# Kernel optimization log

Hardware: AMD Instinct MI355X
Metric: run time of the kernel (lower is better)

## Reference

```python
import jax, jax.numpy as jnp
import numpy as np

B, V, D = 128, 1024, 512

def setup_inputs() -> dict:
    key = jax.random.key(0)
    ks = jax.random.split(key, 6)
    return {
        "features": jax.random.normal(ks[0], (B, D), dtype=jnp.float32),
        "phoneme_counts": jax.random.uniform(ks[1], (V,), minval=0.01, maxval=1.0, dtype=jnp.float32),
        "total_count": jnp.asarray(float(V), dtype=jnp.float32),
        "meg_prototypes": jax.random.normal(ks[2], (V, D), dtype=jnp.float32),
        "zipf_s": jnp.asarray(1.0, dtype=jnp.float32),
        "temperature": jnp.asarray(1.0, dtype=jnp.float32),
        "W1": jax.random.normal(ks[3], (D, 2 * D), dtype=jnp.float32) * 0.02,
        "b1": jnp.zeros((D,), dtype=jnp.float32),
        "W2": jax.random.normal(ks[4], (1, D), dtype=jnp.float32) * 0.02,
        "b2": jnp.zeros((1,), dtype=jnp.float32),
    }

def _l2norm(x, axis=-1, eps=1e-12):
    n = jnp.sqrt(jnp.sum(x * x, axis=axis, keepdims=True))
    return x / jnp.maximum(n, eps)

def reference(features, phoneme_counts, total_count, meg_prototypes,
              zipf_s, temperature, W1, b1, W2, b2):
    vocab = phoneme_counts.shape[0]
    d = features.shape[1]
    # Zipf weights: rank phonemes by frequency (descending), weight = rank^{-s}
    freqs = phoneme_counts / jnp.maximum(total_count, 1.0)
    order = jnp.argsort(-freqs)  # indices sorted by descending frequency
    ranks = jnp.zeros_like(freqs).at[order].set(
        jnp.arange(1, vocab + 1, dtype=freqs.dtype))
    zw = jnp.power(jnp.maximum(ranks, 1.0), -zipf_s)
    zipf_priors = zw / jnp.maximum(zw.sum(), 1e-8)  # [V]
    # Cosine similarity / temperature
    sim = _l2norm(features) @ _l2norm(meg_prototypes).T  # [B, V]
    sim = sim / jnp.maximum(temperature, 1e-4)
    # MLP attention: split Linear(2D,D) into feature and prototype halves,
    # avoiding the materialized [B,V,2D] concat.
    Wf, Wp = W1[:, :d], W1[:, d:]  # each [D, D]
    feat_part = features @ Wf.T          # [B, D]
    proto_part = meg_prototypes @ Wp.T   # [V, D]
    h = jax.nn.relu(feat_part[:, None, :] + proto_part[None, :, :] + b1)  # [B, V, D]
    attn = jax.nn.sigmoid(jnp.einsum('bvd,d->bv', h, W2[0]) + b2[0])      # [B, V]
    weights = zipf_priors[None, :] * (1.0 + sim) * attn
    return jax.nn.softmax(weights, axis=-1)
```

## Files before the change

kernel.cpp:

```cpp
#include <hip/hip_runtime.h>
#include <hip/hip_bf16.h>


typedef __attribute__((ext_vector_type(8))) short bhalf8;
typedef __attribute__((ext_vector_type(4))) float f32x4;

static __device__ __forceinline__ unsigned short f2bf(float x) {
    union { __hip_bfloat16 h; unsigned short u; } cv;
    cv.h = __float2bfloat16(x);
    return cv.u;
}

static __device__ __forceinline__ float bf2f(unsigned short u) {
    return __uint_as_float(((unsigned int)u) << 16);
}

static __device__ __forceinline__ int4 pack_bf16_8(float4 x, float4 y) {
    union { ushort u[8]; int4 v; } r;
    r.u[0] = f2bf(x.x); r.u[1] = f2bf(x.y); r.u[2] = f2bf(x.z); r.u[3] = f2bf(x.w);
    r.u[4] = f2bf(y.x); r.u[5] = f2bf(y.y); r.u[6] = f2bf(y.z); r.u[7] = f2bf(y.w);
    return r.v;
}

__global__ __launch_bounds__(256) void gemm_prep_kernel(
    const float* __restrict__ feat, const float* __restrict__ counts,
    const float* __restrict__ proto, const float* __restrict__ zs,
    const float* __restrict__ W1, const float* __restrict__ b1,
    float* __restrict__ fpT, unsigned short* __restrict__ ppbT,
    float* __restrict__ dotraw,
    float* __restrict__ zw, float* __restrict__ invf, float* __restrict__ invp)
{
    int bx = blockIdx.x, tid = threadIdx.x;

    __shared__ unsigned short As[2][64 * 72];
    __shared__ unsigned short Bs[2][64 * 72];

    if (bx >= 176) {
        if (bx < 192) {
            float* cn = (float*)&As[0][0];
            ((float4*)cn)[tid] = ((const float4*)counts)[tid];
            __syncthreads();
            int il = tid >> 2, q = tid & 3;
            int i = (bx - 176) * 64 + il;
            float ci = cn[i];
            int cnt = 0;
            int j0 = q * 256;
            for (int j = j0; j < j0 + 256; ++j) {
                float cj = cn[j];
                cnt += (cj > ci) ? 1 : 0;
                cnt += (cj == ci && j < i) ? 1 : 0;
            }
            cnt += __shfl_xor(cnt, 1);
            cnt += __shfl_xor(cnt, 2);
            if (q == 0) zw[i] = powf((float)(cnt + 1), -zs[0]);
        } else {
            int nb = bx - 192;
            int w = tid >> 6, lane = tid & 63;
            int row = nb * 4 + w;
            const float* src = (row < 128) ? (feat + (size_t)row * 512)
                                           : (proto + (size_t)(row - 128) * 512);
            const float4* rp = (const float4*)src;
            float4 a = rp[lane * 2], b = rp[lane * 2 + 1];
            float ss = a.x*a.x + a.y*a.y + a.z*a.z + a.w*a.w
                     + b.x*b.x + b.y*b.y + b.z*b.z + b.w*b.w;
            for (int o = 32; o; o >>= 1) ss += __shfl_xor(ss, o);
            if (lane == 0) {
                float inv = 1.0f / fmaxf(sqrtf(ss), 1e-12f);
                if (row < 128) invf[row] = inv; else invp[row - 128] = inv;
            }
        }
        return;
    }

    const float* A; const float* Bm;
    int lda, ldb, tm, tn, mode;
    if (bx < 16) {
        A = feat; lda = 512; Bm = W1; ldb = 1024; mode = 0;
        tm = bx >> 3; tn = bx & 7;
    } else if (bx < 144) {
        int t = bx - 16;
        A = W1 + 512; lda = 1024; Bm = proto; ldb = 512; mode = 1;
        tm = t >> 4; tn = t & 15;
    } else {
        int t = bx - 144;
        A = feat; lda = 512; Bm = proto; ldb = 512; mode = 2;
        tm = t >> 4; tn = t & 15;
    }

    int r = tid >> 2, kq = (tid & 3) * 16;
    int wave = tid >> 6, lane = tid & 63;
    int fr = lane & 15, quad = lane >> 4;

    const float* Ag = A + (size_t)(tm * 64 + r) * lda + kq;
    const float* Bg = Bm + (size_t)(tn * 64 + r) * ldb + kq;

    float4 a0 = *(const float4*)(Ag),      a1 = *(const float4*)(Ag + 4);
    float4 a2 = *(const float4*)(Ag + 8),  a3 = *(const float4*)(Ag + 12);
    float4 g0 = *(const float4*)(Bg),      g1 = *(const float4*)(Bg + 4);
    float4 g2 = *(const float4*)(Bg + 8),  g3 = *(const float4*)(Bg + 12);

    f32x4 acc0 = {0.f, 0.f, 0.f, 0.f};
    f32x4 acc1 = acc0, acc2 = acc0, acc3 = acc0;

    for (int kc = 0; kc < 512; kc += 64) {
        int p = (kc >> 6) & 1;
        *(int4*)&As[p][r * 72 + kq]     = pack_bf16_8(a0, a1);
        *(int4*)&As[p][r * 72 + kq + 8] = pack_bf16_8(a2, a3);
        *(int4*)&Bs[p][r * 72 + kq]     = pack_bf16_8(g0, g1);
        *(int4*)&Bs[p][r * 72 + kq + 8] = pack_bf16_8(g2, g3);
        __syncthreads();
        if (kc + 64 < 512) {
            const float* An = Ag + kc + 64;
            const float* Bn = Bg + kc + 64;
            a0 = *(const float4*)(An);     a1 = *(const float4*)(An + 4);
            a2 = *(const float4*)(An + 8); a3 = *(const float4*)(An + 12);
            g0 = *(const float4*)(Bn);     g1 = *(const float4*)(Bn + 4);
            g2 = *(const float4*)(Bn + 8); g3 = *(const float4*)(Bn + 12);
        }
        #pragma unroll
        for (int s = 0; s < 2; ++s) {
            int ko = s * 32 + quad * 8;
            bhalf8 af  = *(const bhalf8*)&As[p][(wave * 16 + fr) * 72 + ko];
            bhalf8 bf0 = *(const bhalf8*)&Bs[p][(fr) * 72 + ko];
            bhalf8 bf1 = *(const bhalf8*)&Bs[p][(16 + fr) * 72 + ko];
            bhalf8 bf2 = *(const bhalf8*)&Bs[p][(32 + fr) * 72 + ko];
            bhalf8 bf3 = *(const bhalf8*)&Bs[p][(48 + fr) * 72 + ko];
            acc0 = __builtin_amdgcn_mfma_f32_16x16x32_bf16(af, bf0, acc0, 0, 0, 0);
            acc1 = __builtin_amdgcn_mfma_f32_16x16x32_bf16(af, bf1, acc1, 0, 0, 0);
            acc2 = __builtin_amdgcn_mfma_f32_16x16x32_bf16(af, bf2, acc2, 0, 0, 0);
            acc3 = __builtin_amdgcn_mfma_f32_16x16x32_bf16(af, bf3, acc3, 0, 0, 0);
        }
    }

    int m0 = tm * 64 + wave * 16 + quad * 4;
    int n0 = tn * 64 + fr;
    f32x4 accs[4] = {acc0, acc1, acc2, acc3};
    if (mode == 0) {
        for (int j = 0; j < 4; ++j)
            for (int rr = 0; rr < 4; ++rr)
                fpT[(size_t)(n0 + j * 16) * 128 + m0 + rr] = accs[j][rr];
    } else if (mode == 1) {
        float bv4[4];
        for (int rr = 0; rr < 4; ++rr) bv4[rr] = b1[m0 + rr];
        for (int j = 0; j < 4; ++j)
            for (int rr = 0; rr < 4; ++rr)
                ppbT[(size_t)(m0 + rr) * 1024 + n0 + j * 16] = f2bf(accs[j][rr] + bv4[rr]);
    } else {
        for (int j = 0; j < 4; ++j)
            for (int rr = 0; rr < 4; ++rr)
                dotraw[(size_t)(m0 + rr) * 1024 + n0 + j * 16] = accs[j][rr];
    }
}

__global__ __launch_bounds__(1024) void head_kernel(
    const float* __restrict__ fpT, const unsigned short* __restrict__ ppbT,
    const float* __restrict__ dotraw, const float* __restrict__ zw,
    const float* __restrict__ invf, const float* __restrict__ invp,
    const float* __restrict__ temp, const float* __restrict__ W2,
    const float* __restrict__ b2, float* __restrict__ out)
{
    int b = blockIdx.x, tid = threadIdx.x;
    int wave = tid >> 6, lane = tid & 63;
    int vt = tid & 255, ks = tid >> 8;
    int v4 = vt * 4, k0 = ks * 128;

    __shared__ float hpart[4 * 1024];
    __shared__ float red[16];

    float h0 = 0.f, h1 = 0.f, h2 = 0.f, h3 = 0.f;
    const unsigned short* pc = ppbT + v4;
    #pragma unroll 8
    for (int k = k0; k < k0 + 128; ++k) {
        ushort2 u2 = *(const ushort2*)(pc + ((size_t)k << 10));
        unsigned int ua = ((const unsigned int*)&u2)[0];
        unsigned int ub = ((const unsigned int*)&u2)[1];
        float p0 = __uint_as_float(ua << 16);
        float p1 = __uint_as_float(ua & 0xffff0000u);
        float p2 = __uint_as_float(ub << 16);
        float p3 = __uint_as_float(ub & 0xffff0000u);
        float f  = fpT[(size_t)k * 128 + b];
        float w2 = W2[k];
        h0 += fmaxf(f + p0, 0.f) * w2;
        h1 += fmaxf(f + p1, 0.f) * w2;
        h2 += fmaxf(f + p2, 0.f) * w2;
        h3 += fmaxf(f + p3, 0.f) * w2;
    }
    float4 hv = {h0, h1, h2, h3};
    *(float4*)&hpart[ks * 1024 + v4] = hv;

    float zwv = zw[tid];
    float zsl = zwv;
    for (int o = 32; o; o >>= 1) zsl += __shfl_xor(zsl, o);
    if (lane == 0) red[wave] = zsl;
    __syncthreads();
    float zsum = 0.f;
    #pragma unroll
    for (int i = 0; i < 16; ++i) zsum += red[i];
    float izw = 1.0f / fmaxf(zsum, 1e-8f);

    int v = tid;
    float h = hpart[v] + hpart[1024 + v] + hpart[2048 + v] + hpart[3072 + v];

    float it  = invf[b] / fmaxf(temp[0], 1e-4f);
    float sim = dotraw[(size_t)b * 1024 + v] * it * invp[v];
    float w = (zwv * izw) * (1.0f + sim) * (1.0f / (1.0f + expf(-(h + b2[0]))));

    __syncthreads();

    float mx = w;
    for (int o = 32; o; o >>= 1) mx = fmaxf(mx, __shfl_xor(mx, o));
    if (lane == 0) red[wave] = mx;
    __syncthreads();
    mx = red[0];
    #pragma unroll
    for (int i = 1; i < 16; ++i) mx = fmaxf(mx, red[i]);
    __syncthreads();

    float e = expf(w - mx);
    float sm = e;
    for (int o = 32; o; o >>= 1) sm += __shfl_xor(sm, o);
    if (lane == 0) red[wave] = sm;
    __syncthreads();
    float tot = 0.f;
    #pragma unroll
    for (int i = 0; i < 16; ++i) tot += red[i];

    out[(size_t)b * 1024 + v] = e / tot;
}

extern "C" void kernel_launch(void* const* d_in, const int* in_sizes, int n_in,
                              void* d_out, int out_size, void* d_ws, size_t ws_size,
                              hipStream_t stream) {
    const float* feat   = (const float*)d_in[0];
    const float* counts = (const float*)d_in[1];
    const float* proto  = (const float*)d_in[3];
    const float* zs     = (const float*)d_in[4];
    const float* temp   = (const float*)d_in[5];
    const float* W1     = (const float*)d_in[6];
    const float* b1     = (const float*)d_in[7];
    const float* W2     = (const float*)d_in[8];
    const float* b2     = (const float*)d_in[9];

    char* ws = (char*)d_ws;
    float* zw     = (float*)(ws + 0);
    float* invf   = (float*)(ws + 4096);
    float* invp   = (float*)(ws + 4608);
    float* fpT    = (float*)(ws + 8704);
    float* dotraw = (float*)(ws + 270848);
    unsigned short* ppbT = (unsigned short*)(ws + 795136);

    gemm_prep_kernel<<<480, 256, 0, stream>>>(feat, counts, proto, zs, W1, b1,
                                              fpT, ppbT, dotraw, zw, invf, invp);
    head_kernel<<<128, 1024, 0, stream>>>(fpT, ppbT, dotraw, zw, invf, invp,
                                          temp, W2, b2, (float*)d_out);
}
```

Before: 110.2 us.

## Split head into two-block-per-row weight kernel plus separate softmax, coalesce GEMM epilogue

The GEMM epilogue now stages accumulators through shared memory so each thread writes contiguous vectorised float4/int4 chunks instead of scattered scalar stores. The head stage is split: a new kernel uses two blocks per batch row (256 blocks) with 16-way K splitting and 8-wide bf16 vector loads to compute the weights into a workspace buffer. A separate softmax kernel then normalises each row. This raises parallelism and improves memory coalescing, at the cost of an extra kernel launch and an extra round trip of the weight buffer through global memory.

```diff
diff --git a/kernel.cpp b/kernel.cpp
--- a/kernel.cpp
+++ b/kernel.cpp
@@ -9,10 +9,6 @@
     union { __hip_bfloat16 h; unsigned short u; } cv;
     cv.h = __float2bfloat16(x);
     return cv.u;
-}
-
-static __device__ __forceinline__ float bf2f(unsigned short u) {
-    return __uint_as_float(((unsigned int)u) << 16);
 }
 
 static __device__ __forceinline__ int4 pack_bf16_8(float4 x, float4 y) {
@@ -45,6 +41,7 @@
             float ci = cn[i];
             int cnt = 0;
             int j0 = q * 256;
+            #pragma unroll 8
             for (int j = j0; j < j0 + 256; ++j) {
                 float cj = cn[j];
                 cnt += (cj > ci) ? 1 : 0;
@@ -132,64 +129,71 @@
         }
     }
 
-    int m0 = tm * 64 + wave * 16 + quad * 4;
-    int n0 = tn * 64 + fr;
-    f32x4 accs[4] = {acc0, acc1, acc2, acc3};
+    __syncthreads();
+    float* Ct = (float*)&As[0][0];
+    {
+        int rl = wave * 16 + quad * 4;
+        f32x4 accs[4] = {acc0, acc1, acc2, acc3};
+        #pragma unroll
+        for (int j = 0; j < 4; ++j)
+            #pragma unroll
+            for (int rr = 0; rr < 4; ++rr)
+                Ct[(rl + rr) * 65 + fr + j * 16] = accs[j][rr];
+    }
+    __syncthreads();
+
+    int tr = tid >> 2, tq = tid & 3;
     if (mode == 0) {
-        for (int j = 0; j < 4; ++j)
-            for (int rr = 0; rr < 4; ++rr)
-                fpT[(size_t)(n0 + j * 16) * 128 + m0 + rr] = accs[j][rr];
+        float o[16];
+        #pragma unroll
+        for (int i = 0; i < 16; ++i) o[i] = Ct[(tq * 16 + i) * 65 + tr];
+        float* dst = fpT + (size_t)(tn * 64 + tr) * 128 + tm * 64 + tq * 16;
+        #pragma unroll
+        for (int c = 0; c < 4; ++c) {
+            float4 v = {o[c*4], o[c*4+1], o[c*4+2], o[c*4+3]};
+            *(float4*)(dst + c * 4) = v;
+        }
     } else if (mode == 1) {
-        float bv4[4];
-        for (int rr = 0; rr < 4; ++rr) bv4[rr] = b1[m0 + rr];
-        for (int j = 0; j < 4; ++j)
-            for (int rr = 0; rr < 4; ++rr)
-                ppbT[(size_t)(m0 + rr) * 1024 + n0 + j * 16] = f2bf(accs[j][rr] + bv4[rr]);
+        float bv = b1[tm * 64 + tr];
+        float o[16];
+        #pragma unroll
+        for (int i = 0; i < 16; ++i) o[i] = Ct[tr * 65 + tq * 16 + i] + bv;
+        unsigned short* dst = ppbT + (size_t)(tm * 64 + tr) * 1024 + tn * 64 + tq * 16;
+        float4 x0 = {o[0], o[1], o[2], o[3]},   y0 = {o[4], o[5], o[6], o[7]};
+        float4 x1 = {o[8], o[9], o[10], o[11]}, y1 = {o[12], o[13], o[14], o[15]};
+        *(int4*)(dst)     = pack_bf16_8(x0, y0);
+        *(int4*)(dst + 8) = pack_bf16_8(x1, y1);
     } else {
-        for (int j = 0; j < 4; ++j)
-            for (int rr = 0; rr < 4; ++rr)
-                dotraw[(size_t)(m0 + rr) * 1024 + n0 + j * 16] = accs[j][rr];
-    }
-}
-
-__global__ __launch_bounds__(1024) void head_kernel(
+        float* dst = dotraw + (size_t)(tm * 64 + tr) * 1024 + tn * 64 + tq * 16;
+        #pragma unroll
+        for (int c = 0; c < 4; ++c) {
+            float4 v = {Ct[tr * 65 + tq * 16 + c*4],     Ct[tr * 65 + tq * 16 + c*4 + 1],
+                        Ct[tr * 65 + tq * 16 + c*4 + 2], Ct[tr * 65 + tq * 16 + c*4 + 3]};
+            *(float4*)(dst + c * 4) = v;
+        }
+    }
+}
+
+__global__ __launch_bounds__(1024) void head_w_kernel(
     const float* __restrict__ fpT, const unsigned short* __restrict__ ppbT,
     const float* __restrict__ dotraw, const float* __restrict__ zw,
     const float* __restrict__ invf, const float* __restrict__ invp,
     const float* __restrict__ temp, const float* __restrict__ W2,
-    const float* __restrict__ b2, float* __restrict__ out)
+    const float* __restrict__ b2, float* __restrict__ wbuf)
 {
-    int b = blockIdx.x, tid = threadIdx.x;
+    int bx = blockIdx.x, tid = threadIdx.x;
+    int b = bx >> 1, bh = bx & 1;
     int wave = tid >> 6, lane = tid & 63;
-    int vt = tid & 255, ks = tid >> 8;
-    int v4 = vt * 4, k0 = ks * 128;
-
-    __shared__ float hpart[4 * 1024];
+    int vt = tid & 63, ks = tid >> 6;
+    int vl8 = vt * 8;
+    int v8 = bh * 512 + vl8;
+    int k0 = ks * 32;
+
+    __shared__ float hpart[16 * 512];
     __shared__ float red[16];
 
-    float h0 = 0.f, h1 = 0.f, h2 = 0.f, h3 = 0.f;
-    const unsigned short* pc = ppbT + v4;
-    #pragma unroll 8
-    for (int k = k0; k < k0 + 128; ++k) {
-        ushort2 u2 = *(const ushort2*)(pc + ((size_t)k << 10));
-        unsigned int ua = ((const unsigned int*)&u2)[0];
-        unsigned int ub = ((const unsigned int*)&u2)[1];
-        float p0 = __uint_as_float(ua << 16);
-        float p1 = __uint_as_float(ua & 0xffff0000u);
-        float p2 = __uint_as_float(ub << 16);
-        float p3 = __uint_as_float(ub & 0xffff0000u);
-        float f  = fpT[(size_t)k * 128 + b];
-        float w2 = W2[k];
-        h0 += fmaxf(f + p0, 0.f) * w2;
-        h1 += fmaxf(f + p1, 0.f) * w2;
-        h2 += fmaxf(f + p2, 0.f) * w2;
-        h3 += fmaxf(f + p3, 0.f) * w2;
-    }
-    float4 hv = {h0, h1, h2, h3};
-    *(float4*)&hpart[ks * 1024 + v4] = hv;
-
-    float zwv = zw[tid];
-    float zsl = zwv;
+    float zwt = zw[tid];
+    float zsl = zwt;
     for (int o = 32; o; o >>= 1) zsl += __shfl_xor(zsl, o);
     if (lane == 0) red[wave] = zsl;
     __syncthreads();
@@ -198,14 +202,51 @@
     for (int i = 0; i < 16; ++i) zsum += red[i];
     float izw = 1.0f / fmaxf(zsum, 1e-8f);
 
-    int v = tid;
-    float h = hpart[v] + hpart[1024 + v] + hpart[2048 + v] + hpart[3072 + v];
-
-    float it  = invf[b] / fmaxf(temp[0], 1e-4f);
-    float sim = dotraw[(size_t)b * 1024 + v] * it * invp[v];
-    float w = (zwv * izw) * (1.0f + sim) * (1.0f / (1.0f + expf(-(h + b2[0]))));
-
-    __syncthreads();
+    float2 h01 = {0.f, 0.f}, h23 = h01, h45 = h01, h67 = h01;
+    const unsigned short* pc = ppbT + v8;
+    #pragma unroll 8
+    for (int k = k0; k < k0 + 32; ++k) {
+        int4 pv = *(const int4*)(pc + ((size_t)k << 10));
+        unsigned int u0 = (unsigned int)pv.x, u1 = (unsigned int)pv.y;
+        unsigned int u2 = (unsigned int)pv.z, u3 = (unsigned int)pv.w;
+        float f  = fpT[(size_t)k * 128 + b];
+        float w2 = W2[k];
+        float2 p01 = {__uint_as_float(u0 << 16), __uint_as_float(u0 & 0xffff0000u)};
+        float2 p23 = {__uint_as_float(u1 << 16), __uint_as_float(u1 & 0xffff0000u)};
+        float2 p45 = {__uint_as_float(u2 << 16), __uint_as_float(u2 & 0xffff0000u)};
+        float2 p67 = {__uint_as_float(u3 << 16), __uint_as_float(u3 & 0xffff0000u)};
+        h01.x += fmaxf(f + p01.x, 0.f) * w2;  h01.y += fmaxf(f + p01.y, 0.f) * w2;
+        h23.x += fmaxf(f + p23.x, 0.f) * w2;  h23.y += fmaxf(f + p23.y, 0.f) * w2;
+        h45.x += fmaxf(f + p45.x, 0.f) * w2;  h45.y += fmaxf(f + p45.y, 0.f) * w2;
+        h67.x += fmaxf(f + p67.x, 0.f) * w2;  h67.y += fmaxf(f + p67.y, 0.f) * w2;
+    }
+    float4 ha = {h01.x, h01.y, h23.x, h23.y};
+    float4 hb = {h45.x, h45.y, h67.x, h67.y};
+    *(float4*)&hpart[ks * 512 + vl8]     = ha;
+    *(float4*)&hpart[ks * 512 + vl8 + 4] = hb;
+    __syncthreads();
+
+    if (tid < 512) {
+        int vl = tid, v = bh * 512 + vl;
+        float h = 0.f;
+        #pragma unroll
+        for (int s = 0; s < 16; ++s) h += hpart[s * 512 + vl];
+
+        float it  = invf[b] / fmaxf(temp[0], 1e-4f);
+        float sim = dotraw[(size_t)b * 1024 + v] * it * invp[v];
+        float w = (zw[v] * izw) * (1.0f + sim) * (1.0f / (1.0f + expf(-(h + b2[0]))));
+        wbuf[(size_t)b * 1024 + v] = w;
+    }
+}
+
+__global__ __launch_bounds__(1024) void softmax_kernel(
+    const float* __restrict__ wbuf, float* __restrict__ out)
+{
+    int b = blockIdx.x, tid = threadIdx.x;
+    int wave = tid >> 6, lane = tid & 63;
+    __shared__ float red[16];
+
+    float w = wbuf[(size_t)b * 1024 + tid];
 
     float mx = w;
     for (int o = 32; o; o >>= 1) mx = fmaxf(mx, __shfl_xor(mx, o));
@@ -225,7 +266,7 @@
     #pragma unroll
     for (int i = 0; i < 16; ++i) tot += red[i];
 
-    out[(size_t)b * 1024 + v] = e / tot;
+    out[(size_t)b * 1024 + tid] = e / tot;
 }
 
 extern "C" void kernel_launch(void* const* d_in, const int* in_sizes, int n_in,
@@ -248,9 +289,11 @@
     float* fpT    = (float*)(ws + 8704);
     float* dotraw = (float*)(ws + 270848);
     unsigned short* ppbT = (unsigned short*)(ws + 795136);
+    float* wbuf   = (float*)(ws + 1843712);
 
     gemm_prep_kernel<<<480, 256, 0, stream>>>(feat, counts, proto, zs, W1, b1,
                                               fpT, ppbT, dotraw, zw, invf, invp);
-    head_kernel<<<128, 1024, 0, stream>>>(fpT, ppbT, dotraw, zw, invf, invp,
-                                          temp, W2, b2, (float*)d_out);
-}
+    head_w_kernel<<<256, 1024, 0, stream>>>(fpT, ppbT, dotraw, zw, invf, invp,
+                                            temp, W2, b2, wbuf);
+    softmax_kernel<<<128, 1024, 0, stream>>>(wbuf, (float*)d_out);
+}
```

After: 102.6 us. 6.9% less time.
